# Kernel optimization log

Hardware: AMD Instinct MI355X
Metric: run time of the kernel (lower is better)

## Reference

```python
import jax, jax.numpy as jnp
import numpy as np

LEN_HIS = 20   # q_len_his: sliding-window history length
DIM_C = 4      # dim_c
H = 64         # GRU hidden = final_mlp_hidden_width
D = 36         # global_graph_width(32) + goal(2) + action(2)
N = 32768      # total timesteps across many episodes


def setup_inputs() -> dict:
    key = jax.random.key(0)
    ks = jax.random.split(key, 8)
    emb = jax.random.normal(ks[0], (N, D), jnp.float32)
    dones = (jax.random.uniform(ks[1], (N, 1)) < 0.02).astype(jnp.int32)
    s = lambda k, shape, fan: jax.random.normal(k, shape, jnp.float32) / np.sqrt(fan).astype(np.float32)
    return {
        "embeddings": emb,
        "W_ih": s(ks[2], (3 * H, D), D),
        "W_hh": s(ks[3], (3 * H, H), H),
        "b_ih": jnp.zeros((3 * H,), jnp.float32),
        "b_hh": jnp.zeros((3 * H,), jnp.float32),
        "W1": s(ks[4], (H, H), H),
        "b1": jnp.zeros((H,), jnp.float32),
        "W2": s(ks[5], (DIM_C, H), H),
        "b2": jnp.zeros((DIM_C,), jnp.float32),
        "dones": dones,
    }


def _his_calculate_c(embeddings, W_ih, W_hh, b_ih, b_hh, W1, b1, W2, b2, dones):
    """Batched/padded version of the ragged sliding-window GRU+MLP loop.

    For each timestep t, the torch code runs the GRU over
    embeddings[max(episode_start, t-L+1) : t+1] from a zero hidden state,
    then applies FinalPredMLP to the final hidden state.
    """
    n = embeddings.shape[0]
    done = dones[:, 0] != 0
    idx = jnp.arange(n)
    # episode_start[t] = (index of most recent done strictly before t) + 1, else 0
    prev_done = jnp.concatenate([jnp.zeros((1,), bool), done[:-1]])
    ep_start = jax.lax.cummax(jnp.where(prev_done, idx, 0))
    win_start = jnp.maximum(ep_start, idx - LEN_HIS + 1)            # [N]

    # padded windows: position l holds embeddings[t - (L-1) + l]
    gidx = idx[:, None] - (LEN_HIS - 1) + jnp.arange(LEN_HIS)[None, :]  # [N, L]
    valid = gidx >= win_start[:, None]                                   # [N, L]
    X = embeddings[jnp.clip(gidx, 0, n - 1)] * valid[..., None]          # [N, L, D]

    def cell(h, inp):
        x, v = inp                      # x: [N, D], v: [N]
        gi = x @ W_ih.T + b_ih          # [N, 3H]
        gh = h @ W_hh.T + b_hh          # [N, 3H]
        ir, iz, inn = jnp.split(gi, 3, axis=-1)
        hr, hz, hnn = jnp.split(gh, 3, axis=-1)
        r = jax.nn.sigmoid(ir + hr)
        z = jax.nn.sigmoid(iz + hz)
        ncand = jnp.tanh(inn + r * hnn)
        h_new = (1.0 - z) * ncand + z * h
        return jnp.where(v[:, None], h_new, h), None

    h0 = jnp.zeros((n, H), embeddings.dtype)
    hT, _ = jax.lax.scan(cell, h0, (jnp.swapaxes(X, 0, 1), valid.T))  # [N, H]

    # FinalPredMLP: Linear(H,H) -> ReLU -> Linear(H, dim_c)
    hid = jax.nn.relu(hT @ W1.T + b1)
    return hid @ W2.T + b2              # [N, dim_c]


def reference(embeddings, W_ih, W_hh, b_ih, b_hh, W1, b1, W2, b2, dones):
    return _his_calculate_c(embeddings, W_ih, W_hh, b_ih, b_hh, W1, b1, W2, b2, dones)
```

## Files before the change

kernel.cpp:

```cpp
#include <hip/hip_runtime.h>

#define NT 32768
#define DI 36
#define HH 64
#define LH 20
#define TPB 64
#define NROW 83
#define SGS 196
#define EMBS 40

#define NLOG2E -1.4426950408889634f
#define TLOG2E 2.8853900817779268f

#define UNION_OFF  65072
#define SFIRST_OFF 78352
#define SMEM_BYTES 78608

typedef __attribute__((ext_vector_type(8))) short bf16x8;
typedef __attribute__((ext_vector_type(4))) float f32x4;
typedef __attribute__((ext_vector_type(4))) int int4v;
union frag_cast { int4v i4; bf16x8 h8; };

__device__ __forceinline__ unsigned f2u(float f) { union { float f; unsigned u; } x; x.f = f; return x.u; }
__device__ __forceinline__ float u2f(unsigned u) { union { float f; unsigned u; } x; x.u = u; return x.f; }
__device__ __forceinline__ unsigned short f2bf_rne(float f) {
    union { float f; unsigned u; } x; x.f = f;
    unsigned r = x.u + 0x7FFFu + ((x.u >> 16) & 1u);
    return (unsigned short)(r >> 16);
}

__global__ __launch_bounds__(64) void prep_kernel(
    const float* __restrict__ W_ih, const float* __restrict__ W_hh,
    const float* __restrict__ W1, int4v* __restrict__ wfrag)
{
    const int b = (int)blockIdx.x;
    const int l = (int)threadIdx.x;
    unsigned short e[8];
    if (b < 72) {
        const int set = b / 24, fb = b % 24;
        const int mt = fb >> 1, kt = fb & 1;
        const int m = mt * 16 + (l & 15);
        const float sc = ((mt >> 2) < 2) ? NLOG2E : TLOG2E;
        const int k0 = kt * 32 + (l >> 4) * 8;
#pragma unroll
        for (int jj = 0; jj < 8; ++jj) {
            const int k = k0 + jj;
            if (set == 2) {
                e[jj] = f2bf_rne(W_hh[(size_t)m * HH + k] * sc);
            } else {
                const float v = (k < DI) ? W_ih[(size_t)m * DI + k] * sc : 0.f;
                const unsigned u = f2u(v);
                if (set == 0) e[jj] = (unsigned short)(u >> 16);
                else          e[jj] = (unsigned short)(f2u(v - u2f(u & 0xFFFF0000u)) >> 16);
            }
        }
    } else {
        const int bb = b - 72;
        const bool is_lo = bb >= 8;
        const int f = bb & 7;
        const int mt = f >> 1, kt = f & 1;
        const int m = mt * 16 + (l & 15);
        const int k0 = kt * 32 + (l >> 4) * 8;
#pragma unroll
        for (int jj = 0; jj < 8; ++jj) {
            const float v = W1[(size_t)m * HH + k0 + jj];
            const unsigned u = f2u(v);
            if (!is_lo) e[jj] = (unsigned short)(u >> 16);
            else        e[jj] = (unsigned short)(f2u(v - u2f(u & 0xFFFF0000u)) >> 16);
        }
    }
    int4v p;
    p.x = e[0] | ((unsigned)e[1] << 16); p.y = e[2] | ((unsigned)e[3] << 16);
    p.z = e[4] | ((unsigned)e[5] << 16); p.w = e[6] | ((unsigned)e[7] << 16);
    wfrag[b * 64 + l] = p;
}

__global__ __launch_bounds__(256, 2) void gru_kernel(
    const float* __restrict__ emb, const int4v* __restrict__ wfrag,
    const float* __restrict__ b_ih, const float* __restrict__ b_hh,
    const float* __restrict__ b1, const float* __restrict__ W2,
    const float* __restrict__ b2, const int* __restrict__ dones,
    float* __restrict__ out)
{
    __shared__ __align__(16) char SMEM[SMEM_BYTES];
    float* const Sg = (float*)SMEM;
    unsigned short* const EmbH = (unsigned short*)(SMEM + UNION_OFF);
    unsigned short* const EmbL = EmbH + NROW * EMBS;
    unsigned short* const Hb   = (unsigned short*)(SMEM + UNION_OFF);
    int* const sfirst = (int*)(SMEM + SFIRST_OFF);

    const int tid = threadIdx.x;
    const int lane = tid & 63;
    const int W = tid >> 6;
    const int li = lane & 15;
    const int q = lane >> 4;
    const int blk = ((int)blockIdx.x & 7) * 64 + ((int)blockIdx.x >> 3);
    const int T0 = blk * TPB;

    {
        int4v* z = (int4v*)EmbH;
        for (int i = tid; i < 830; i += 256) z[i] = int4v{0, 0, 0, 0};
    }
    if (tid < TPB) {
        const int tt = T0 + tid;
        int lo = tt - (LH - 1); if (lo < 0) lo = 0;
        int ws = lo;
        for (int j = lo; j < tt; ++j)
            ws = (dones[j] != 0) ? (j + 1) : ws;
        sfirst[tid] = ws - (tt - (LH - 1));
    }
    __syncthreads();
    for (int i = tid; i < NROW * DI; i += 256) {
        const int r = i / DI, c = i % DI;
        int tt = T0 - (LH - 1) + r; tt = tt < 0 ? 0 : tt;
        const float v = emb[(size_t)tt * DI + c];
        const unsigned u = f2u(v);
        EmbH[r * EMBS + c] = (unsigned short)(u >> 16);
        EmbL[r * EMBS + c] = (unsigned short)(f2u(v - u2f(u & 0xFFFF0000u)) >> 16);
    }

    bf16x8 aih[3][2], ail[3][2];
#pragma unroll
    for (int g = 0; g < 3; ++g)
#pragma unroll
        for (int kt = 0; kt < 2; ++kt) {
            const int fb = (4 * g + W) * 2 + kt;
            frag_cast a, b;
            a.i4 = wfrag[(0 * 24 + fb) * 64 + lane];
            b.i4 = wfrag[(1 * 24 + fb) * 64 + lane];
            aih[g][kt] = a.h8; ail[g][kt] = b.h8;
        }

    const int joff = 16 * W + 4 * q;
    f32x4 biasI[3];
#pragma unroll
    for (int g = 0; g < 3; ++g) {
        const float sc = (g < 2) ? NLOG2E : TLOG2E;
        const f32x4 bi = *(const f32x4*)&b_ih[64 * g + joff];
        if (g < 2) {
            const f32x4 bh = *(const f32x4*)&b_hh[64 * g + joff];
#pragma unroll
            for (int rr = 0; rr < 4; ++rr) biasI[g][rr] = (bi[rr] + bh[rr]) * sc;
        } else {
#pragma unroll
            for (int rr = 0; rr < 4; ++rr) biasI[g][rr] = bi[rr] * sc;
        }
    }
    __syncthreads();

#pragma unroll
    for (int rt = 0; rt < 6; ++rt) {
        const int row0 = (rt == 5) ? 67 : 16 * rt;
        const int row = row0 + li;
        bf16x8 ebh0 = *(const bf16x8*)&EmbH[row * EMBS + 8 * q];
        bf16x8 ebl0 = *(const bf16x8*)&EmbL[row * EMBS + 8 * q];
        bf16x8 ebh1 = bf16x8{0, 0, 0, 0, 0, 0, 0, 0};
        bf16x8 ebl1 = bf16x8{0, 0, 0, 0, 0, 0, 0, 0};
        if (q == 0) {
            ebh1 = *(const bf16x8*)&EmbH[row * EMBS + 32];
            ebl1 = *(const bf16x8*)&EmbL[row * EMBS + 32];
        }
#pragma unroll
        for (int g = 0; g < 3; ++g) {
            f32x4 a = biasI[g];
            a = __builtin_amdgcn_mfma_f32_16x16x32_bf16(aih[g][0], ebh0, a, 0, 0, 0);
            a = __builtin_amdgcn_mfma_f32_16x16x32_bf16(aih[g][1], ebh1, a, 0, 0, 0);
            a = __builtin_amdgcn_mfma_f32_16x16x32_bf16(ail[g][0], ebh0, a, 0, 0, 0);
            a = __builtin_amdgcn_mfma_f32_16x16x32_bf16(ail[g][1], ebh1, a, 0, 0, 0);
            a = __builtin_amdgcn_mfma_f32_16x16x32_bf16(aih[g][0], ebl0, a, 0, 0, 0);
            a = __builtin_amdgcn_mfma_f32_16x16x32_bf16(aih[g][1], ebl1, a, 0, 0, 0);
            *(f32x4*)&Sg[row * SGS + 64 * g + joff] = a;
        }
    }
    __syncthreads();

    bf16x8 whh[3][4][2];
#pragma unroll
    for (int g = 0; g < 3; ++g)
#pragma unroll
        for (int mt = 0; mt < 4; ++mt)
#pragma unroll
            for (int kt = 0; kt < 2; ++kt) {
                frag_cast c;
                c.i4 = wfrag[(48 + (4 * g + mt) * 2 + kt) * 64 + lane];
                whh[g][mt][kt] = c.h8;
            }
    f32x4 bnv4[4];
#pragma unroll
    for (int mt = 0; mt < 4; ++mt) {
        const f32x4 b = *(const f32x4*)&b_hh[128 + 16 * mt + 4 * q];
#pragma unroll
        for (int rr = 0; rr < 4; ++rr) bnv4[mt][rr] = b[rr] * TLOG2E;
    }
    const int sfr = sfirst[16 * W + li];
    unsigned short* const Hbw = Hb + W * 1152;

    float h[4][4];
    {
        const float* gp = Sg + (16 * W + li) * SGS;
        const bool valid = (0 >= sfr);
#pragma unroll
        for (int mt = 0; mt < 4; ++mt) {
            const f32x4 aR = *(const f32x4*)(gp + 16 * mt + 4 * q);
            const f32x4 aZ = *(const f32x4*)(gp + 64 + 16 * mt + 4 * q);
            const f32x4 gI = *(const f32x4*)(gp + 128 + 16 * mt + 4 * q);
#pragma unroll
            for (int rr = 0; rr < 4; ++rr) {
                const float r  = __builtin_amdgcn_rcpf(1.f + __builtin_amdgcn_exp2f(aR[rr]));
                const float z  = __builtin_amdgcn_rcpf(1.f + __builtin_amdgcn_exp2f(aZ[rr]));
                const float nc = 1.f - 2.f * __builtin_amdgcn_rcpf(1.f + __builtin_amdgcn_exp2f(gI[rr] + r * bnv4[mt][rr]));
                h[mt][rr] = valid ? fmaf(z, 0.f - nc, nc) : 0.f;
            }
            uint2 ph;
            ph.x = __builtin_amdgcn_perm(f2u(h[mt][1]), f2u(h[mt][0]), 0x07060302u);
            ph.y = __builtin_amdgcn_perm(f2u(h[mt][3]), f2u(h[mt][2]), 0x07060302u);
            *(uint2*)&Hbw[li * 72 + 16 * mt + 4 * q] = ph;
        }
    }

#pragma unroll 1
    for (int s = 1; s < LH; ++s) {
        const bf16x8 bh0 = *(const bf16x8*)&Hbw[li * 72 + 8 * q];
        const bf16x8 bh1 = *(const bf16x8*)&Hbw[li * 72 + 32 + 8 * q];
        const float* gp = Sg + (16 * W + li + s) * SGS;
        f32x4 aR[4], aZ[4], aN[4], gI[4];
#pragma unroll
        for (int mt = 0; mt < 4; ++mt) {
            aR[mt] = *(const f32x4*)(gp + 16 * mt + 4 * q);
            aZ[mt] = *(const f32x4*)(gp + 64 + 16 * mt + 4 * q);
            gI[mt] = *(const f32x4*)(gp + 128 + 16 * mt + 4 * q);
            aN[mt] = bnv4[mt];
        }
#pragma unroll
        for (int mt = 0; mt < 4; ++mt) {
            aR[mt] = __builtin_amdgcn_mfma_f32_16x16x32_bf16(whh[0][mt][0], bh0, aR[mt], 0, 0, 0);
            aR[mt] = __builtin_amdgcn_mfma_f32_16x16x32_bf16(whh[0][mt][1], bh1, aR[mt], 0, 0, 0);
            aZ[mt] = __builtin_amdgcn_mfma_f32_16x16x32_bf16(whh[1][mt][0], bh0, aZ[mt], 0, 0, 0);
            aZ[mt] = __builtin_amdgcn_mfma_f32_16x16x32_bf16(whh[1][mt][1], bh1, aZ[mt], 0, 0, 0);
            aN[mt] = __builtin_amdgcn_mfma_f32_16x16x32_bf16(whh[2][mt][0], bh0, aN[mt], 0, 0, 0);
            aN[mt] = __builtin_amdgcn_mfma_f32_16x16x32_bf16(whh[2][mt][1], bh1, aN[mt], 0, 0, 0);
        }
        const bool valid = (s >= sfr);
#pragma unroll
        for (int mt = 0; mt < 4; ++mt) {
#pragma unroll
            for (int rr = 0; rr < 4; ++rr) {
                const float r  = __builtin_amdgcn_rcpf(1.f + __builtin_amdgcn_exp2f(aR[mt][rr]));
                const float z  = __builtin_amdgcn_rcpf(1.f + __builtin_amdgcn_exp2f(aZ[mt][rr]));
                const float nc = 1.f - 2.f * __builtin_amdgcn_rcpf(1.f + __builtin_amdgcn_exp2f(gI[mt][rr] + r * aN[mt][rr]));
                const float hn = fmaf(z, h[mt][rr] - nc, nc);
                h[mt][rr] = valid ? hn : h[mt][rr];
            }
            if (s != LH - 1) {
                uint2 ph;
                ph.x = __builtin_amdgcn_perm(f2u(h[mt][1]), f2u(h[mt][0]), 0x07060302u);
                ph.y = __builtin_amdgcn_perm(f2u(h[mt][3]), f2u(h[mt][2]), 0x07060302u);
                *(uint2*)&Hbw[li * 72 + 16 * mt + 4 * q] = ph;
            }
        }
    }

    bf16x8 w1h[4][2], w1l[4][2];
#pragma unroll
    for (int mt = 0; mt < 4; ++mt)
#pragma unroll
        for (int kt = 0; kt < 2; ++kt) {
            frag_cast a, b;
            a.i4 = wfrag[(72 + mt * 2 + kt) * 64 + lane];
            b.i4 = wfrag[(80 + mt * 2 + kt) * 64 + lane];
            w1h[mt][kt] = a.h8; w1l[mt][kt] = b.h8;
        }
#pragma unroll
    for (int mt = 0; mt < 4; ++mt) {
        uint2 ph;
        ph.x = __builtin_amdgcn_perm(f2u(h[mt][1]), f2u(h[mt][0]), 0x07060302u);
        ph.y = __builtin_amdgcn_perm(f2u(h[mt][3]), f2u(h[mt][2]), 0x07060302u);
        *(uint2*)&Hbw[li * 72 + 16 * mt + 4 * q] = ph;
    }
    const bf16x8 bh0 = *(const bf16x8*)&Hbw[li * 72 + 8 * q];
    const bf16x8 bh1 = *(const bf16x8*)&Hbw[li * 72 + 32 + 8 * q];
#pragma unroll
    for (int mt = 0; mt < 4; ++mt) {
        const unsigned u0 = f2u(h[mt][0]), u1 = f2u(h[mt][1]);
        const unsigned u2 = f2u(h[mt][2]), u3 = f2u(h[mt][3]);
        const unsigned l0 = f2u(h[mt][0] - u2f(u0 & 0xFFFF0000u));
        const unsigned l1 = f2u(h[mt][1] - u2f(u1 & 0xFFFF0000u));
        const unsigned l2 = f2u(h[mt][2] - u2f(u2 & 0xFFFF0000u));
        const unsigned l3 = f2u(h[mt][3] - u2f(u3 & 0xFFFF0000u));
        uint2 pl;
        pl.x = __builtin_amdgcn_perm(l1, l0, 0x07060302u);
        pl.y = __builtin_amdgcn_perm(l3, l2, 0x07060302u);
        *(uint2*)&Hbw[li * 72 + 16 * mt + 4 * q] = pl;
    }
    const bf16x8 bl0 = *(const bf16x8*)&Hbw[li * 72 + 8 * q];
    const bf16x8 bl1 = *(const bf16x8*)&Hbw[li * 72 + 32 + 8 * q];

    float p0 = 0.f, p1 = 0.f, p2 = 0.f, p3 = 0.f;
#pragma unroll
    for (int mt = 0; mt < 4; ++mt) {
        f32x4 a = *(const f32x4*)&b1[16 * mt + 4 * q];
        a = __builtin_amdgcn_mfma_f32_16x16x32_bf16(w1h[mt][0], bh0, a, 0, 0, 0);
        a = __builtin_amdgcn_mfma_f32_16x16x32_bf16(w1h[mt][1], bh1, a, 0, 0, 0);
        a = __builtin_amdgcn_mfma_f32_16x16x32_bf16(w1l[mt][0], bh0, a, 0, 0, 0);
        a = __builtin_amdgcn_mfma_f32_16x16x32_bf16(w1l[mt][1], bh1, a, 0, 0, 0);
        a = __builtin_amdgcn_mfma_f32_16x16x32_bf16(w1h[mt][0], bl0, a, 0, 0, 0);
        a = __builtin_amdgcn_mfma_f32_16x16x32_bf16(w1h[mt][1], bl1, a, 0, 0, 0);
        const float h0 = fmaxf(a[0], 0.f), h1 = fmaxf(a[1], 0.f);
        const float h2 = fmaxf(a[2], 0.f), h3 = fmaxf(a[3], 0.f);
        const f32x4 w0 = *(const f32x4*)&W2[0 * HH + 16 * mt + 4 * q];
        const f32x4 w1 = *(const f32x4*)&W2[1 * HH + 16 * mt + 4 * q];
        const f32x4 w2 = *(const f32x4*)&W2[2 * HH + 16 * mt + 4 * q];
        const f32x4 w3 = *(const f32x4*)&W2[3 * HH + 16 * mt + 4 * q];
        p0 += h0 * w0[0] + h1 * w0[1] + h2 * w0[2] + h3 * w0[3];
        p1 += h0 * w1[0] + h1 * w1[1] + h2 * w1[2] + h3 * w1[3];
        p2 += h0 * w2[0] + h1 * w2[1] + h2 * w2[2] + h3 * w2[3];
        p3 += h0 * w3[0] + h1 * w3[1] + h2 * w3[2] + h3 * w3[3];
    }
    p0 += __shfl_xor(p0, 16); p0 += __shfl_xor(p0, 32);
    p1 += __shfl_xor(p1, 16); p1 += __shfl_xor(p1, 32);
    p2 += __shfl_xor(p2, 16); p2 += __shfl_xor(p2, 32);
    p3 += __shfl_xor(p3, 16); p3 += __shfl_xor(p3, 32);
    const float pv = (q == 0) ? p0 : (q == 1) ? p1 : (q == 2) ? p2 : p3;
    out[(size_t)(T0 + 16 * W + li) * 4 + q] = pv + b2[q];
}

extern "C" void kernel_launch(void* const* d_in, const int* in_sizes, int n_in,
                              void* d_out, int out_size, void* d_ws, size_t ws_size,
                              hipStream_t stream) {
    const float* emb  = (const float*)d_in[0];
    const float* W_ih = (const float*)d_in[1];
    const float* W_hh = (const float*)d_in[2];
    const float* b_ih = (const float*)d_in[3];
    const float* b_hh = (const float*)d_in[4];
    const float* W1   = (const float*)d_in[5];
    const float* b1   = (const float*)d_in[6];
    const float* W2   = (const float*)d_in[7];
    const float* b2   = (const float*)d_in[8];
    const int*   dn   = (const int*)d_in[9];

    int4v* wfrag = (int4v*)d_ws;
    float* o = (float*)d_out;

    prep_kernel<<<88, 64, 0, stream>>>(W_ih, W_hh, W1, wfrag);
    gru_kernel<<<NT / TPB, 256, 0, stream>>>(emb, wfrag, b_ih, b_hh,
                                             b1, W2, b2, dn, o);
}
```

Baseline: 112.4 us.

## Batch reciprocals in GRU gates, prefetch next-step gate inputs, vectorize embedding load

Adds a gate4 helper that computes four sigmoids with one shared reciprocal, using products of the denominators, so three rcp calls replace twelve per tile. It prefetches the next step's input-gate rows from LDS into registers, unrolls the recurrence loop by two, and interleaves the gate math with the MFMA issue for each tile. The prologue computes sfirst with an unrolled scan, loads embeddings as float4 with packed bf16 hi/lo stores, zeroes only the pad columns, drops one barrier, and hoists the W_hh fragment loads earlier. Multiplying four denominators together can overflow or underflow when gate inputs are large, and the extra live registers may reduce occupancy.

```diff
diff --git a/kernel.cpp b/kernel.cpp
--- a/kernel.cpp
+++ b/kernel.cpp
@@ -27,6 +27,46 @@
     union { float f; unsigned u; } x; x.f = f;
     unsigned r = x.u + 0x7FFFu + ((x.u >> 16) & 1u);
     return (unsigned short)(r >> 16);
+}
+
+__device__ __forceinline__ void gate4(const f32x4 aR, const f32x4 aZ,
+                                      const f32x4 aI, const f32x4 aN,
+                                      const bool valid, float* hh) {
+    float dR[4], dZ[4], dN[4], rv[4], zv[4], iv[4];
+#pragma unroll
+    for (int e = 0; e < 4; ++e) dR[e] = 1.f + __builtin_amdgcn_exp2f(aR[e]);
+#pragma unroll
+    for (int e = 0; e < 4; ++e) dZ[e] = 1.f + __builtin_amdgcn_exp2f(aZ[e]);
+    {
+        const float pa = dR[0] * dR[1], pb = dR[2] * dR[3];
+        const float rp = __builtin_amdgcn_rcpf(pa * pb);
+        const float ia = rp * pb, ib = rp * pa;
+        rv[0] = ia * dR[1]; rv[1] = ia * dR[0];
+        rv[2] = ib * dR[3]; rv[3] = ib * dR[2];
+    }
+    {
+        const float pa = dZ[0] * dZ[1], pb = dZ[2] * dZ[3];
+        const float rp = __builtin_amdgcn_rcpf(pa * pb);
+        const float ia = rp * pb, ib = rp * pa;
+        zv[0] = ia * dZ[1]; zv[1] = ia * dZ[0];
+        zv[2] = ib * dZ[3]; zv[3] = ib * dZ[2];
+    }
+#pragma unroll
+    for (int e = 0; e < 4; ++e)
+        dN[e] = 1.f + __builtin_amdgcn_exp2f(fmaf(rv[e], aN[e], aI[e]));
+    {
+        const float pa = dN[0] * dN[1], pb = dN[2] * dN[3];
+        const float rp = __builtin_amdgcn_rcpf(pa * pb);
+        const float ia = rp * pb, ib = rp * pa;
+        iv[0] = ia * dN[1]; iv[1] = ia * dN[0];
+        iv[2] = ib * dN[3]; iv[3] = ib * dN[2];
+    }
+#pragma unroll
+    for (int e = 0; e < 4; ++e) {
+        const float nc = fmaf(-2.f, iv[e], 1.f);
+        const float hn = fmaf(zv[e], hh[e] - nc, nc);
+        hh[e] = valid ? hn : hh[e];
+    }
 }
 
 __global__ __launch_bounds__(64) void prep_kernel(
@@ -97,26 +137,40 @@
     const int blk = ((int)blockIdx.x & 7) * 64 + ((int)blockIdx.x >> 3);
     const int T0 = blk * TPB;
 
-    {
-        int4v* z = (int4v*)EmbH;
-        for (int i = tid; i < 830; i += 256) z[i] = int4v{0, 0, 0, 0};
-    }
     if (tid < TPB) {
         const int tt = T0 + tid;
-        int lo = tt - (LH - 1); if (lo < 0) lo = 0;
-        int ws = lo;
-        for (int j = lo; j < tt; ++j)
-            ws = (dones[j] != 0) ? (j + 1) : ws;
-        sfirst[tid] = ws - (tt - (LH - 1));
-    }
-    __syncthreads();
-    for (int i = tid; i < NROW * DI; i += 256) {
-        const int r = i / DI, c = i % DI;
+        int off = (tt >= LH - 1) ? 0 : (LH - 1) - tt;
+#pragma unroll
+        for (int k = LH - 1; k >= 1; --k) {
+            const int j = tt - k;
+            const int jj = j < 0 ? 0 : j;
+            const bool d = (j >= 0) && (dones[jj] != 0);
+            if (d) off = LH - k;
+        }
+        sfirst[tid] = off;
+    }
+    for (int i = tid; i < NROW * 9; i += 256) {
+        const int r = i / 9, c = i - r * 9;
         int tt = T0 - (LH - 1) + r; tt = tt < 0 ? 0 : tt;
-        const float v = emb[(size_t)tt * DI + c];
-        const unsigned u = f2u(v);
-        EmbH[r * EMBS + c] = (unsigned short)(u >> 16);
-        EmbL[r * EMBS + c] = (unsigned short)(f2u(v - u2f(u & 0xFFFF0000u)) >> 16);
+        const f32x4 v = *(const f32x4*)&emb[(size_t)tt * DI + 4 * c];
+        const unsigned u0 = f2u(v[0]), u1 = f2u(v[1]);
+        const unsigned u2 = f2u(v[2]), u3 = f2u(v[3]);
+        uint2 ph, pl;
+        ph.x = __builtin_amdgcn_perm(u1, u0, 0x07060302u);
+        ph.y = __builtin_amdgcn_perm(u3, u2, 0x07060302u);
+        const unsigned l0 = f2u(v[0] - u2f(u0 & 0xFFFF0000u));
+        const unsigned l1 = f2u(v[1] - u2f(u1 & 0xFFFF0000u));
+        const unsigned l2 = f2u(v[2] - u2f(u2 & 0xFFFF0000u));
+        const unsigned l3 = f2u(v[3] - u2f(u3 & 0xFFFF0000u));
+        pl.x = __builtin_amdgcn_perm(l1, l0, 0x07060302u);
+        pl.y = __builtin_amdgcn_perm(l3, l2, 0x07060302u);
+        *(uint2*)&EmbH[r * EMBS + 4 * c] = ph;
+        *(uint2*)&EmbL[r * EMBS + 4 * c] = pl;
+    }
+    if (tid < NROW) {
+        const uint2 z2 = {0u, 0u};
+        *(uint2*)&EmbH[tid * EMBS + DI] = z2;
+        *(uint2*)&EmbL[tid * EMBS + DI] = z2;
     }
 
     bf16x8 aih[3][2], ail[3][2];
@@ -130,6 +184,17 @@
             b.i4 = wfrag[(1 * 24 + fb) * 64 + lane];
             aih[g][kt] = a.h8; ail[g][kt] = b.h8;
         }
+    bf16x8 whh[3][4][2];
+#pragma unroll
+    for (int g = 0; g < 3; ++g)
+#pragma unroll
+        for (int mt = 0; mt < 4; ++mt)
+#pragma unroll
+            for (int kt = 0; kt < 2; ++kt) {
+                frag_cast c;
+                c.i4 = wfrag[(48 + (4 * g + mt) * 2 + kt) * 64 + lane];
+                whh[g][mt][kt] = c.h8;
+            }
 
     const int joff = 16 * W + 4 * q;
     f32x4 biasI[3];
@@ -174,17 +239,6 @@
     }
     __syncthreads();
 
-    bf16x8 whh[3][4][2];
-#pragma unroll
-    for (int g = 0; g < 3; ++g)
-#pragma unroll
-        for (int mt = 0; mt < 4; ++mt)
-#pragma unroll
-            for (int kt = 0; kt < 2; ++kt) {
-                frag_cast c;
-                c.i4 = wfrag[(48 + (4 * g + mt) * 2 + kt) * 64 + lane];
-                whh[g][mt][kt] = c.h8;
-            }
     f32x4 bnv4[4];
 #pragma unroll
     for (int mt = 0; mt < 4; ++mt) {
@@ -196,6 +250,7 @@
     unsigned short* const Hbw = Hb + W * 1152;
 
     float h[4][4];
+    f32x4 gvR[4], gvZ[4], gvI[4];
     {
         const float* gp = Sg + (16 * W + li) * SGS;
         const bool valid = (0 >= sfr);
@@ -203,34 +258,43 @@
         for (int mt = 0; mt < 4; ++mt) {
             const f32x4 aR = *(const f32x4*)(gp + 16 * mt + 4 * q);
             const f32x4 aZ = *(const f32x4*)(gp + 64 + 16 * mt + 4 * q);
-            const f32x4 gI = *(const f32x4*)(gp + 128 + 16 * mt + 4 * q);
-#pragma unroll
-            for (int rr = 0; rr < 4; ++rr) {
-                const float r  = __builtin_amdgcn_rcpf(1.f + __builtin_amdgcn_exp2f(aR[rr]));
-                const float z  = __builtin_amdgcn_rcpf(1.f + __builtin_amdgcn_exp2f(aZ[rr]));
-                const float nc = 1.f - 2.f * __builtin_amdgcn_rcpf(1.f + __builtin_amdgcn_exp2f(gI[rr] + r * bnv4[mt][rr]));
-                h[mt][rr] = valid ? fmaf(z, 0.f - nc, nc) : 0.f;
-            }
+            const f32x4 aI = *(const f32x4*)(gp + 128 + 16 * mt + 4 * q);
+            h[mt][0] = 0.f; h[mt][1] = 0.f; h[mt][2] = 0.f; h[mt][3] = 0.f;
+            gate4(aR, aZ, aI, bnv4[mt], valid, h[mt]);
             uint2 ph;
             ph.x = __builtin_amdgcn_perm(f2u(h[mt][1]), f2u(h[mt][0]), 0x07060302u);
             ph.y = __builtin_amdgcn_perm(f2u(h[mt][3]), f2u(h[mt][2]), 0x07060302u);
             *(uint2*)&Hbw[li * 72 + 16 * mt + 4 * q] = ph;
         }
-    }
-
-#pragma unroll 1
+        const float* gq = Sg + (16 * W + li + 1) * SGS;
+#pragma unroll
+        for (int mt = 0; mt < 4; ++mt) {
+            gvR[mt] = *(const f32x4*)(gq + 16 * mt + 4 * q);
+            gvZ[mt] = *(const f32x4*)(gq + 64 + 16 * mt + 4 * q);
+            gvI[mt] = *(const f32x4*)(gq + 128 + 16 * mt + 4 * q);
+        }
+    }
+
+#pragma unroll 2
     for (int s = 1; s < LH; ++s) {
         const bf16x8 bh0 = *(const bf16x8*)&Hbw[li * 72 + 8 * q];
         const bf16x8 bh1 = *(const bf16x8*)&Hbw[li * 72 + 32 + 8 * q];
-        const float* gp = Sg + (16 * W + li + s) * SGS;
-        f32x4 aR[4], aZ[4], aN[4], gI[4];
+        f32x4 aR[4], aZ[4], aN[4], aI[4];
 #pragma unroll
         for (int mt = 0; mt < 4; ++mt) {
-            aR[mt] = *(const f32x4*)(gp + 16 * mt + 4 * q);
-            aZ[mt] = *(const f32x4*)(gp + 64 + 16 * mt + 4 * q);
-            gI[mt] = *(const f32x4*)(gp + 128 + 16 * mt + 4 * q);
-            aN[mt] = bnv4[mt];
-        }
+            aR[mt] = gvR[mt]; aZ[mt] = gvZ[mt]; aI[mt] = gvI[mt]; aN[mt] = bnv4[mt];
+        }
+        {
+            int rrow = 16 * W + li + s + 1; rrow = rrow > NROW - 1 ? NROW - 1 : rrow;
+            const float* gq = Sg + rrow * SGS;
+#pragma unroll
+            for (int mt = 0; mt < 4; ++mt) {
+                gvR[mt] = *(const f32x4*)(gq + 16 * mt + 4 * q);
+                gvZ[mt] = *(const f32x4*)(gq + 64 + 16 * mt + 4 * q);
+                gvI[mt] = *(const f32x4*)(gq + 128 + 16 * mt + 4 * q);
+            }
+        }
+        const bool valid = (s >= sfr);
 #pragma unroll
         for (int mt = 0; mt < 4; ++mt) {
             aR[mt] = __builtin_amdgcn_mfma_f32_16x16x32_bf16(whh[0][mt][0], bh0, aR[mt], 0, 0, 0);
@@ -239,18 +303,7 @@
             aZ[mt] = __builtin_amdgcn_mfma_f32_16x16x32_bf16(whh[1][mt][1], bh1, aZ[mt], 0, 0, 0);
             aN[mt] = __builtin_amdgcn_mfma_f32_16x16x32_bf16(whh[2][mt][0], bh0, aN[mt], 0, 0, 0);
             aN[mt] = __builtin_amdgcn_mfma_f32_16x16x32_bf16(whh[2][mt][1], bh1, aN[mt], 0, 0, 0);
-        }
-        const bool valid = (s >= sfr);
-#pragma unroll
-        for (int mt = 0; mt < 4; ++mt) {
-#pragma unroll
-            for (int rr = 0; rr < 4; ++rr) {
-                const float r  = __builtin_amdgcn_rcpf(1.f + __builtin_amdgcn_exp2f(aR[mt][rr]));
-                const float z  = __builtin_amdgcn_rcpf(1.f + __builtin_amdgcn_exp2f(aZ[mt][rr]));
-                const float nc = 1.f - 2.f * __builtin_amdgcn_rcpf(1.f + __builtin_amdgcn_exp2f(gI[mt][rr] + r * aN[mt][rr]));
-                const float hn = fmaf(z, h[mt][rr] - nc, nc);
-                h[mt][rr] = valid ? hn : h[mt][rr];
-            }
+            gate4(aR[mt], aZ[mt], aI[mt], aN[mt], valid, h[mt]);
             if (s != LH - 1) {
                 uint2 ph;
                 ph.x = __builtin_amdgcn_perm(f2u(h[mt][1]), f2u(h[mt][0]), 0x07060302u);
```

New measurement: 111.4 us. About the same (-0.9%).
